# Kernel tuning notes

Hardware: AMD Instinct MI355X
Metric: run time of the kernel (lower is better)

Reference implementation:

```python
import jax, jax.numpy as jnp
import numpy as np

N = 8192
H_CHANNELS = 2048
HEADS = 16
D = H_CHANNELS // HEADS  # 128


def setup_inputs() -> dict:
    key = jax.random.key(0)
    k1, k2, k3 = jax.random.split(key, 3)
    x0 = jax.random.normal(k1, (N, H_CHANNELS), dtype=jnp.float32)
    # boolean mask: True entries are masked out (set to -inf)
    mask = jax.random.randint(k2, (N, N), 0, 2).astype(jnp.bool_)
    # torch Linear weight layout: [out_features, in_features] = [3*d, h_channels]
    W_qkv = jax.random.normal(k3, (3 * D, H_CHANNELS), dtype=jnp.float32) * (1.0 / np.sqrt(H_CHANNELS))
    return {"x0": x0, "mask": mask, "W_qkv": W_qkv}


def reference(x0, mask, W_qkv):
    # qkv = x0 @ W^T : [N, 3d]
    qkv = x0 @ W_qkv.T
    q, k, v = jnp.split(qkv, 3, axis=-1)          # each [N, d]
    att_logits = (q @ k.T) / D                    # [N, N]  (note: scale is /d, not /sqrt(d))
    att_logits = jnp.where(mask, -jnp.inf, att_logits)
    att = jax.nn.softmax(att_logits, axis=-1)     # [N, N]
    # dropout p=0.0 (eval mode) -> identity
    return att @ v                                # [N, d]
```

## Files before the change

### kernel.cpp

```cpp
#include <hip/hip_runtime.h>
#include <hip/hip_bf16.h>

typedef __attribute__((ext_vector_type(8))) short short8;
typedef __attribute__((ext_vector_type(4))) float f32x4;

#define NTOK 8192
#define HCH  2048
#define DDIM 128
#define NSPLIT 8
#define KPS   (NTOK / NSPLIT)
#define NITER (KPS / 64)

__device__ __forceinline__ unsigned short f2bf(float f) {
    __hip_bfloat16 h = __float2bfloat16(f);
    return *reinterpret_cast<unsigned short*>(&h);
}
__device__ __forceinline__ unsigned short f2h(float f) {
    _Float16 h = (_Float16)f;
    return *reinterpret_cast<unsigned short*>(&h);
}

__global__ void detect_kernel(const unsigned int* __restrict__ X,
                              const unsigned int* __restrict__ M,
                              int* __restrict__ flags)
{
    const int lane = threadIdx.x & 63;
    unsigned int e = (X[lane] >> 7) & 0xFF;
    unsigned long long hb = __ballot(e >= 110 && e <= 140);

    bool w_ok = true, h_ok = true, b_ok = true;
#pragma unroll
    for (int i = 0; i < 16; i++) {
        unsigned int u = M[lane + 64 * i];
        if (!(u == 0u || u == 1u || u == 0x3F800000u)) w_ok = false;
        unsigned int h0 = u & 0xFFFFu, h1 = u >> 16;
        bool o0 = (h0 == 0u || h0 == 0x3F80u || h0 == 0x3C00u || h0 == 1u);
        bool o1 = (h1 == 0u || h1 == 0x3F80u || h1 == 0x3C00u || h1 == 1u);
        if (!(o0 && o1)) h_ok = false;
        unsigned int b0 = u & 0xFF, b1 = (u >> 8) & 0xFF,
                     b2 = (u >> 16) & 0xFF, b3 = u >> 24;
        if (b0 > 1u || b1 > 1u || b2 > 1u || b3 > 1u) b_ok = false;
    }
    bool allw = __all(w_ok), allh = __all(h_ok), allb = __all(b_ok);
    if (lane == 0) {
        flags[0] = (__popcll(hb) < 32) ? 1 : 0;
        flags[1] = allw ? 0 : (allb ? 1 : (allh ? 2 : 3));
    }
}

__global__ __launch_bounds__(256) void conv_w(
    const void* __restrict__ Wv, const int* __restrict__ flags,
    unsigned short* __restrict__ Wbf)
{
    int t = blockIdx.x * 256 + threadIdx.x;
    size_t off = (size_t)t * 8;
    if (flags[0] != 0) {
        const float* Wf = (const float*)Wv;
        float4 a = *reinterpret_cast<const float4*>(Wf + off);
        float4 b = *reinterpret_cast<const float4*>(Wf + off + 4);
        unsigned short o[8] = { f2bf(a.x), f2bf(a.y), f2bf(a.z), f2bf(a.w),
                                f2bf(b.x), f2bf(b.y), f2bf(b.z), f2bf(b.w) };
        *reinterpret_cast<uint4*>(Wbf + off) = *reinterpret_cast<uint4*>(o);
    } else {
        *reinterpret_cast<uint4*>(Wbf + off) =
            *reinterpret_cast<const uint4*>((const unsigned short*)Wv + off);
    }
}

__global__ __launch_bounds__(256) void mask_pack(
    const void* __restrict__ maskv, const int* __restrict__ flags,
    unsigned char* __restrict__ Mp)
{
    const int mmode = flags[1];
    const int NB = NTOK * (NTOK / 8);
    int t0 = blockIdx.x * 256 + threadIdx.x;
    for (int b = t0; b < NB; b += 2048 * 256) {
        unsigned int byte = 0;
        if (mmode == 0) {
            const uint4* p = reinterpret_cast<const uint4*>(
                (const unsigned int*)maskv + (size_t)b * 8);
            uint4 a = p[0], c = p[1];
            byte = (a.x != 0u) | ((a.y != 0u) << 1) | ((a.z != 0u) << 2) | ((a.w != 0u) << 3)
                 | ((c.x != 0u) << 4) | ((c.y != 0u) << 5) | ((c.z != 0u) << 6) | ((c.w != 0u) << 7);
        } else if (mmode == 1) {
            unsigned long long v = *reinterpret_cast<const unsigned long long*>(
                (const unsigned char*)maskv + (size_t)b * 8);
#pragma unroll
            for (int k = 0; k < 8; k++)
                byte |= (((v >> (8 * k)) & 0xFFull) != 0ull) << k;
        } else if (mmode == 2) {
            uint4 a = *reinterpret_cast<const uint4*>(
                (const unsigned short*)maskv + (size_t)b * 8);
            byte = ((a.x & 0xFFFFu) != 0u) | ((a.x >> 16 != 0u) << 1)
                 | (((a.y & 0xFFFFu) != 0u) << 2) | ((a.y >> 16 != 0u) << 3)
                 | (((a.z & 0xFFFFu) != 0u) << 4) | ((a.z >> 16 != 0u) << 5)
                 | (((a.w & 0xFFFFu) != 0u) << 6) | ((a.w >> 16 != 0u) << 7);
        } else {
            byte = ((const unsigned char*)maskv)[b];
        }
        Mp[b] = (unsigned char)byte;
    }
}

__global__ __launch_bounds__(256) void qkv_gemm(
    const void* __restrict__ Xv, const unsigned short* __restrict__ Wbf,
    const int* __restrict__ flags,
    unsigned short* __restrict__ Qb, unsigned short* __restrict__ Kb,
    unsigned short* __restrict__ Vb)
{
    __shared__ unsigned short Wsm[128 * 64];
    __shared__ unsigned short Xsm[32 * 64];
    const int tid  = threadIdx.x;
    const int lane = tid & 63, w = tid >> 6;
    const int c = lane & 15, g = lane >> 4;
    const int q0 = blockIdx.x * 32;
    const int n0 = blockIdx.y * 128;
    const bool f32in = (flags[0] != 0);
    const float*          Xf = (const float*)Xv;
    const unsigned short* Xb = (const unsigned short*)Xv;

    f32x4 acc[4];
#pragma unroll
    for (int i = 0; i < 4; i++) acc[i] = (f32x4){0.f, 0.f, 0.f, 0.f};

    const int xrow = tid >> 3, xc8 = tid & 7;
    const int arow = (w & 1) * 16 + c;

    for (int kk = 0; kk < HCH; kk += 64) {
        __syncthreads();
#pragma unroll
        for (int i = 0; i < 4; i++) {
            int cid = tid + 256 * i;
            int n = cid >> 3, c8 = cid & 7;
            uint4 v = *reinterpret_cast<const uint4*>(Wbf + (size_t)(n0 + n) * HCH + kk + c8 * 8);
            *reinterpret_cast<uint4*>(&Wsm[(n * 8 + (c8 ^ (n & 7))) * 8]) = v;
        }
        {
            unsigned short o[8];
            if (f32in) {
                const float* p = Xf + (size_t)(q0 + xrow) * HCH + kk + xc8 * 8;
                float4 a = *reinterpret_cast<const float4*>(p);
                float4 b = *reinterpret_cast<const float4*>(p + 4);
                o[0]=f2bf(a.x); o[1]=f2bf(a.y); o[2]=f2bf(a.z); o[3]=f2bf(a.w);
                o[4]=f2bf(b.x); o[5]=f2bf(b.y); o[6]=f2bf(b.z); o[7]=f2bf(b.w);
            } else {
                *reinterpret_cast<uint4*>(o) =
                    *reinterpret_cast<const uint4*>(Xb + (size_t)(q0 + xrow) * HCH + kk + xc8 * 8);
            }
            *reinterpret_cast<uint4*>(&Xsm[(xrow * 8 + (xc8 ^ (xrow & 7))) * 8]) =
                *reinterpret_cast<uint4*>(o);
        }
        __syncthreads();
#pragma unroll
        for (int ks = 0; ks < 2; ks++) {
            short8 af = *reinterpret_cast<const short8*>(
                &Xsm[(arow * 8 + ((ks * 4 + g) ^ (c & 7))) * 8]);
#pragma unroll
            for (int nt = 0; nt < 4; nt++) {
                int n = (w >> 1) * 64 + nt * 16 + c;
                short8 bf = *reinterpret_cast<const short8*>(
                    &Wsm[(n * 8 + ((ks * 4 + g) ^ (c & 7))) * 8]);
                acc[nt] = __builtin_amdgcn_mfma_f32_16x16x32_bf16(af, bf, acc[nt], 0, 0, 0);
            }
        }
    }
    unsigned short* dst = (blockIdx.y == 0) ? Qb : (blockIdx.y == 1) ? Kb : Vb;
#pragma unroll
    for (int nt = 0; nt < 4; nt++) {
        int n = (w >> 1) * 64 + nt * 16 + c;
#pragma unroll
        for (int r = 0; r < 4; r++) {
            int rr = q0 + (w & 1) * 16 + g * 4 + r;
            dst[(size_t)rr * DDIM + n] = f2bf(acc[nt][r]);
        }
    }
}

__global__ __launch_bounds__(256) void vtrans(
    const unsigned short* __restrict__ V, unsigned short* __restrict__ VT)
{
    __shared__ unsigned short T[32 * 33];
    const int t = threadIdx.x;
    const int k0 = blockIdx.x * 32, d0 = blockIdx.y * 32;
    {
        int key = t >> 3, dq = (t & 7) * 4;
        ushort4 v = *reinterpret_cast<const ushort4*>(V + (size_t)(k0 + key) * DDIM + d0 + dq);
        T[(dq + 0) * 33 + key] = v.x;
        T[(dq + 1) * 33 + key] = v.y;
        T[(dq + 2) * 33 + key] = v.z;
        T[(dq + 3) * 33 + key] = v.w;
    }
    __syncthreads();
    {
        int d = t >> 3, kq = (t & 7) * 4;
        ushort4 o;
        o.x = T[d * 33 + kq + 0]; o.y = T[d * 33 + kq + 1];
        o.z = T[d * 33 + kq + 2]; o.w = T[d * 33 + kq + 3];
        *reinterpret_cast<ushort4*>(VT + (size_t)(d0 + d) * NTOK + k0 + kq) = o;
    }
}

__global__ __launch_bounds__(256) void attn_part(
    const unsigned short* __restrict__ Qb, const unsigned short* __restrict__ Kb,
    const unsigned short* __restrict__ VT, const unsigned long long* __restrict__ Mp,
    _Float16* __restrict__ Opart, float* __restrict__ lpart)
{
    __shared__ unsigned short Ksm[64 * 128];
    __shared__ unsigned short Vsm[128 * 64];
    __shared__ unsigned short Psm[4 * 16 * 64];
    const int tid  = threadIdx.x;
    const int lane = tid & 63, w = tid >> 6;
    const int c = lane & 15, g = lane >> 4;
    const int split = blockIdx.x;
    const int qb    = blockIdx.y;
    const int q0 = qb * 128;
    const int kbase = split * KPS;
    const int tb0 = kbase >> 6;
    unsigned short* Pw = &Psm[w * 16 * 64];

    short8 qf[2][4];
#pragma unroll
    for (int rt = 0; rt < 2; rt++)
#pragma unroll
        for (int ks = 0; ks < 4; ks++)
            qf[rt][ks] = *reinterpret_cast<const short8*>(
                Qb + (size_t)(q0 + w * 32 + rt * 16 + c) * DDIM + ks * 32 + g * 8);

    short8 ones;
#pragma unroll
    for (int i = 0; i < 8; i++) ones[i] = (short)0x3F80;

    f32x4 accO[2][8];
#pragma unroll
    for (int rt = 0; rt < 2; rt++)
#pragma unroll
        for (int i = 0; i < 8; i++) accO[rt][i] = (f32x4){0.f, 0.f, 0.f, 0.f};
    f32x4 accL[2] = {(f32x4){0.f,0.f,0.f,0.f}, (f32x4){0.f,0.f,0.f,0.f}};

    unsigned long long mp[2][4], mpn[2][4];
#pragma unroll
    for (int rt = 0; rt < 2; rt++)
#pragma unroll
        for (int r = 0; r < 4; r++)
            mp[rt][r] = Mp[(size_t)(q0 + w * 32 + rt * 16 + g * 4 + r) * 128 + tb0];

    for (int t = 0; t < NITER; t++) {
        const int k0 = kbase + t * 64;
        __syncthreads();
#pragma unroll
        for (int i = 0; i < 4; i++) {
            int cid = tid + 256 * i;
            int rowk = cid >> 4, c16 = cid & 15;
            uint4 v = *reinterpret_cast<const uint4*>(Kb + (size_t)(k0 + rowk) * DDIM + c16 * 8);
            *reinterpret_cast<uint4*>(&Ksm[(rowk * 16 + (c16 ^ (rowk & 15))) * 8]) = v;
        }
#pragma unroll
        for (int i = 0; i < 4; i++) {
            int cid = tid + 256 * i;
            int d = cid >> 3, c8 = cid & 7;
            uint4 v = *reinterpret_cast<const uint4*>(VT + (size_t)d * NTOK + k0 + c8 * 8);
            *reinterpret_cast<uint4*>(&Vsm[(d * 8 + (c8 ^ (d & 7))) * 8]) = v;
        }
        if (t + 1 < NITER) {
#pragma unroll
            for (int rt = 0; rt < 2; rt++)
#pragma unroll
                for (int r = 0; r < 4; r++)
                    mpn[rt][r] = Mp[(size_t)(q0 + w * 32 + rt * 16 + g * 4 + r) * 128 + tb0 + t + 1];
        }
        __syncthreads();

#pragma unroll
        for (int rt = 0; rt < 2; rt++) {
            f32x4 sacc[4];
#pragma unroll
            for (int nt = 0; nt < 4; nt++) {
                sacc[nt] = (f32x4){0.f, 0.f, 0.f, 0.f};
#pragma unroll
                for (int ks = 0; ks < 4; ks++) {
                    short8 bf = *reinterpret_cast<const short8*>(
                        &Ksm[((nt * 16 + c) * 16 + ((ks * 4 + g) ^ c)) * 8]);
                    sacc[nt] = __builtin_amdgcn_mfma_f32_16x16x32_bf16(qf[rt][ks], bf, sacc[nt], 0, 0, 0);
                }
            }
#pragma unroll
            for (int nt = 0; nt < 4; nt++)
#pragma unroll
                for (int r = 0; r < 4; r++) {
                    bool mv = (mp[rt][r] >> (nt * 16 + c)) & 1ull;
                    float p = mv ? 0.f : __expf(sacc[nt][r] * (1.0f / 128.0f));
                    int row = g * 4 + r;
                    Pw[(row * 8 + ((nt * 2 + (c >> 3)) ^ (row & 7))) * 8 + (c & 7)] = f2bf(p);
                }
#pragma unroll
            for (int ks2 = 0; ks2 < 2; ks2++) {
                short8 af = *reinterpret_cast<const short8*>(
                    &Pw[(c * 8 + ((ks2 * 4 + g) ^ (c & 7))) * 8]);
                accL[rt] = __builtin_amdgcn_mfma_f32_16x16x32_bf16(af, ones, accL[rt], 0, 0, 0);
#pragma unroll
                for (int dt = 0; dt < 8; dt++) {
                    short8 bfv = *reinterpret_cast<const short8*>(
                        &Vsm[((dt * 16 + c) * 8 + ((ks2 * 4 + g) ^ (c & 7))) * 8]);
                    accO[rt][dt] = __builtin_amdgcn_mfma_f32_16x16x32_bf16(af, bfv, accO[rt][dt], 0, 0, 0);
                }
            }
        }
#pragma unroll
        for (int rt = 0; rt < 2; rt++)
#pragma unroll
            for (int r = 0; r < 4; r++) mp[rt][r] = mpn[rt][r];
    }

    _Float16* Ob = Opart + ((size_t)split * 64 + qb) * (128 * DDIM) + (size_t)w * 4096;
#pragma unroll
    for (int rt = 0; rt < 2; rt++)
#pragma unroll
        for (int r = 0; r < 4; r++) {
            unsigned short o[8];
#pragma unroll
            for (int dt = 0; dt < 8; dt++) o[dt] = f2h(accO[rt][dt][r]);
            *reinterpret_cast<uint4*>(Ob + ((((rt * 4 + r) * 4 + g) * 16 + c) * 8)) =
                *reinterpret_cast<uint4*>(o);
        }
    if (c == 0) {
#pragma unroll
        for (int rt = 0; rt < 2; rt++)
#pragma unroll
            for (int r = 0; r < 4; r++)
                lpart[(size_t)split * NTOK + q0 + w * 32 + rt * 16 + g * 4 + r] = accL[rt][r];
    }
}

__global__ __launch_bounds__(256) void combine(
    const _Float16* __restrict__ Opart, const float* __restrict__ lpart,
    float* __restrict__ out)
{
    int idx = blockIdx.x * 256 + threadIdx.x;
    int row = idx >> 7, d = idx & 127;
    int qb = row >> 7, win = row & 127;
    int w = win >> 5, rt = (win >> 4) & 1, g = (win >> 2) & 3, r = win & 3;
    int nt = d >> 4, c = d & 15;
    size_t off = (size_t)qb * (128 * DDIM) + (size_t)w * 4096
               + ((((rt * 4 + r) * 4 + g) * 16 + c) * 8) + nt;
    const size_t S = (size_t)NTOK * DDIM;
    float den = 0.f, num = 0.f;
#pragma unroll
    for (int s = 0; s < NSPLIT; s++) {
        den += lpart[(size_t)s * NTOK + row];
        num += (float)Opart[(size_t)s * S + off];
    }
    out[idx] = (den > 0.f) ? (num / den) : 0.f;
}

extern "C" void kernel_launch(void* const* d_in, const int* in_sizes, int n_in,
                              void* d_out, int out_size, void* d_ws, size_t ws_size,
                              hipStream_t stream)
{
    const void* X = d_in[0]; const void* mask = d_in[1]; const void* W = d_in[2];
    {
        const void* x_ = nullptr; const void* m_ = nullptr; const void* w_ = nullptr;
        for (int i = 0; i < n_in; i++) {
            if (in_sizes[i] == 16777216) x_ = d_in[i];
            else if (in_sizes[i] == 67108864) m_ = d_in[i];
            else if (in_sizes[i] == 786432) w_ = d_in[i];
        }
        if (x_ && m_ && w_) { X = x_; mask = m_; W = w_; }
    }
    float* out = (float*)d_out;

    char* ws = (char*)d_ws;
    unsigned short* Qb  = (unsigned short*)(ws);
    unsigned short* Kb  = (unsigned short*)(ws + (2ull << 20));
    unsigned short* VT  = (unsigned short*)(ws + (4ull << 20));
    unsigned long long* Mpk = (unsigned long long*)(ws + (6ull << 20));
    _Float16*       Opart = (_Float16*)(ws + (14ull << 20));
    unsigned short* Wbf = (unsigned short*)(ws + (14ull << 20));
    unsigned short* Vb  = (unsigned short*)(ws + (14ull << 20) + (1536ull << 10));
    float*          lpart = (float*)(ws + (30ull << 20));
    int*            flags = (int*)(ws + (30ull << 20) + (512ull << 10));

    detect_kernel<<<1, 64, 0, stream>>>((const unsigned int*)X, (const unsigned int*)mask, flags);
    conv_w<<<dim3(384), 256, 0, stream>>>(W, flags, Wbf);
    mask_pack<<<dim3(2048), 256, 0, stream>>>(mask, flags, (unsigned char*)Mpk);
    qkv_gemm<<<dim3(256, 3), 256, 0, stream>>>(X, Wbf, flags, Qb, Kb, Vb);
    vtrans<<<dim3(256, 4), 256, 0, stream>>>(Vb, VT);
    attn_part<<<dim3(NSPLIT, 64), 256, 0, stream>>>(Qb, Kb, VT, Mpk, Opart, lpart);
    combine<<<dim3(4096), 256, 0, stream>>>(Opart, lpart, out);
}
```

Measured before the change: 543.8 us.

## Double-buffer K/V tiles with direct global-to-LDS async loads

```diff
diff --git a/kernel.cpp b/kernel.cpp
--- a/kernel.cpp
+++ b/kernel.cpp
@@ -18,6 +18,15 @@
 __device__ __forceinline__ unsigned short f2h(float f) {
     _Float16 h = (_Float16)f;
     return *reinterpret_cast<unsigned short*>(&h);
+}
+
+__device__ __forceinline__ void gload_lds16(const void* g, void* l) {
+    __builtin_amdgcn_global_load_lds(
+        reinterpret_cast<const __attribute__((address_space(1))) unsigned int*>(
+            reinterpret_cast<uintptr_t>(g)),
+        reinterpret_cast<__attribute__((address_space(3))) unsigned int*>(
+            reinterpret_cast<uintptr_t>(l)),
+        16, 0, 0);
 }
 
 __global__ void detect_kernel(const unsigned int* __restrict__ X,
@@ -205,8 +214,8 @@
     const unsigned short* __restrict__ VT, const unsigned long long* __restrict__ Mp,
     _Float16* __restrict__ Opart, float* __restrict__ lpart)
 {
-    __shared__ unsigned short Ksm[64 * 128];
-    __shared__ unsigned short Vsm[128 * 64];
+    __shared__ unsigned short Ksm[2][64 * 128];
+    __shared__ unsigned short Vsm[2][128 * 64];
     __shared__ unsigned short Psm[4 * 16 * 64];
     const int tid  = threadIdx.x;
     const int lane = tid & 63, w = tid >> 6;
@@ -218,6 +227,24 @@
     const int tb0 = kbase >> 6;
     unsigned short* Pw = &Psm[w * 16 * 64];
 
+    auto stage = [&](int b, int tt) {
+        const int k0s = kbase + tt * 64;
+#pragma unroll
+        for (int i = 0; i < 4; i++) {
+            int cid = tid + 256 * i;
+            int rowk = cid >> 4, c16 = cid & 15;
+            gload_lds16(Kb + (size_t)(k0s + rowk) * DDIM + ((c16 ^ (rowk & 15)) * 8),
+                        &Ksm[b][cid * 8]);
+        }
+#pragma unroll
+        for (int i = 0; i < 4; i++) {
+            int cid = tid + 256 * i;
+            int d = cid >> 3, c8 = cid & 7;
+            gload_lds16(VT + (size_t)d * NTOK + k0s + ((c8 ^ (d & 7)) * 8),
+                        &Vsm[b][cid * 8]);
+        }
+    };
+
     short8 qf[2][4];
 #pragma unroll
     for (int rt = 0; rt < 2; rt++)
@@ -244,31 +271,20 @@
         for (int r = 0; r < 4; r++)
             mp[rt][r] = Mp[(size_t)(q0 + w * 32 + rt * 16 + g * 4 + r) * 128 + tb0];
 
+    stage(0, 0);
+
     for (int t = 0; t < NITER; t++) {
-        const int k0 = kbase + t * 64;
         __syncthreads();
-#pragma unroll
-        for (int i = 0; i < 4; i++) {
-            int cid = tid + 256 * i;
-            int rowk = cid >> 4, c16 = cid & 15;
-            uint4 v = *reinterpret_cast<const uint4*>(Kb + (size_t)(k0 + rowk) * DDIM + c16 * 8);
-            *reinterpret_cast<uint4*>(&Ksm[(rowk * 16 + (c16 ^ (rowk & 15))) * 8]) = v;
-        }
-#pragma unroll
-        for (int i = 0; i < 4; i++) {
-            int cid = tid + 256 * i;
-            int d = cid >> 3, c8 = cid & 7;
-            uint4 v = *reinterpret_cast<const uint4*>(VT + (size_t)d * NTOK + k0 + c8 * 8);
-            *reinterpret_cast<uint4*>(&Vsm[(d * 8 + (c8 ^ (d & 7))) * 8]) = v;
-        }
         if (t + 1 < NITER) {
+            stage((t + 1) & 1, t + 1);
 #pragma unroll
             for (int rt = 0; rt < 2; rt++)
 #pragma unroll
                 for (int r = 0; r < 4; r++)
                     mpn[rt][r] = Mp[(size_t)(q0 + w * 32 + rt * 16 + g * 4 + r) * 128 + tb0 + t + 1];
         }
-        __syncthreads();
+        const unsigned short* Ks = Ksm[t & 1];
+        const unsigned short* Vs = Vsm[t & 1];
 
 #pragma unroll
         for (int rt = 0; rt < 2; rt++) {
@@ -279,7 +295,7 @@
 #pragma unroll
                 for (int ks = 0; ks < 4; ks++) {
                     short8 bf = *reinterpret_cast<const short8*>(
-                        &Ksm[((nt * 16 + c) * 16 + ((ks * 4 + g) ^ c)) * 8]);
+                        &Ks[((nt * 16 + c) * 16 + ((ks * 4 + g) ^ c)) * 8]);
                     sacc[nt] = __builtin_amdgcn_mfma_f32_16x16x32_bf16(qf[rt][ks], bf, sacc[nt], 0, 0, 0);
                 }
             }
@@ -300,7 +316,7 @@
 #pragma unroll
                 for (int dt = 0; dt < 8; dt++) {
                     short8 bfv = *reinterpret_cast<const short8*>(
-                        &Vsm[((dt * 16 + c) * 8 + ((ks2 * 4 + g) ^ (c & 7))) * 8]);
+                        &Vs[((dt * 16 + c) * 8 + ((ks2 * 4 + g) ^ (c & 7))) * 8]);
                     accO[rt][dt] = __builtin_amdgcn_mfma_f32_16x16x32_bf16(af, bfv, accO[rt][dt], 0, 0, 0);
                 }
             }
```

After: 541.6 us. Within noise of the previous version (-0.4%).
